# Performance work log

Hardware: AMD Instinct MI355X
Metric: run time of the kernel (lower is better)

The kernel has to match this reference:

```python
import jax, jax.numpy as jnp
import numpy as np


def _kernelize(data, projection_matrix):
    # FAVOR+ positive softmax features: ratio * h(x) * f(x @ P^T)
    # h(x) = exp(-||x||^2 / 2), f(u) = exp(u)
    d = data.shape[-1]
    r = projection_matrix.shape[0]
    data_norm = (d ** -0.25) * data                       # [n, d]
    ratio = r ** -0.5
    data_dash = jnp.einsum('id,rd->ir', data_norm, projection_matrix)  # [n, r]
    h = jnp.exp(-0.5 * jnp.sum(data_norm * data_norm, axis=-1, keepdims=True))  # [n, 1]
    return ratio * h * jnp.exp(data_dash)                 # [n, r]


def setup_inputs() -> dict:
    key = jax.random.key(0)
    k1, k2, k3, k4 = jax.random.split(key, 4)
    n, d, dv, r = 65536, 64, 64, 256
    q = jax.random.normal(k1, (n, d), dtype=jnp.float32)
    k = jax.random.normal(k2, (n, d), dtype=jnp.float32)
    v = jax.random.normal(k3, (n, dv), dtype=jnp.float32)
    projection_matrix = jax.random.normal(k4, (r, d), dtype=jnp.float32)
    return {"q": q, "k": k, "v": v, "projection_matrix": projection_matrix}


def reference(q, k, v, projection_matrix):
    q_hat = _kernelize(q, projection_matrix)              # [n, r]
    k_hat = _kernelize(k, projection_matrix)              # [n, r]
    z = k_hat.T @ v                                       # [r, dv]  (FAVOR associativity)
    w = q_hat @ z                                         # [n, dv]
    d_inv = 1.0 / jnp.sum(q_hat * jnp.sum(k_hat, axis=0), axis=1, keepdims=True)  # [n, 1]
    return d_inv * w
```

## Files before the change

### kernel.cpp

```cpp
#include <hip/hip_runtime.h>
#include <math.h>

typedef __attribute__((ext_vector_type(8))) short bf16x8;
typedef __attribute__((ext_vector_type(4))) short bf16x4;
typedef __attribute__((ext_vector_type(4))) float f32x4;

#define NROWS 65536
#define RFEAT 256
#define PARTN 20480
#define NGROUP 16

#define OFF_PB 0
#define OFF_ZB 32768
#define OFF_P2 73728
#define OFF_VB 1384448
#define OFF_PARTIALS 9773056

#define SC 0.35355339059327373f
#define LNRATIO -2.772588722239781f

__device__ __forceinline__ unsigned short f2bf(float f) {
    union { float f; unsigned int u; } v; v.f = f;
    unsigned int r = v.u + 0x7FFFu + ((v.u >> 16) & 1u);
    return (unsigned short)(r >> 16);
}

__global__ __launch_bounds__(256)
void prep_kernel(const float* __restrict__ V, const float* __restrict__ P,
                 unsigned short* __restrict__ Vb, unsigned short* __restrict__ Pb)
{
    const int t = threadIdx.x;
    if (blockIdx.x == 1024) {
        const int l = t & 63, g = t >> 6;
        for (int f = g * 8; f < g * 8 + 8; f++) {
            const int kstep = f >> 4, nt = f & 15;
            const float* src = P + (nt * 16 + (l & 15)) * 64 + kstep * 32 + (l >> 4) * 8;
            bf16x8 frag;
            #pragma unroll
            for (int j = 0; j < 8; j++) frag[j] = (short)f2bf(SC * src[j]);
            *(bf16x8*)(Pb + f * 512 + l * 8) = frag;
        }
        return;
    }
    __shared__ unsigned short vl[64 * 68];
    const int row = t >> 2, c0 = (t & 3) * 16;
    const float4* src = (const float4*)(V + ((size_t)blockIdx.x * 64 + row) * 64 + c0);
    unsigned short* dst = vl + row * 68 + c0;
    #pragma unroll
    for (int jj = 0; jj < 4; jj++) {
        float4 a = src[jj];
        dst[4*jj+0] = f2bf(a.x); dst[4*jj+1] = f2bf(a.y);
        dst[4*jj+2] = f2bf(a.z); dst[4*jj+3] = f2bf(a.w);
    }
    __syncthreads();
    const int l = t & 63;
    #pragma unroll
    for (int h = 0; h < 2; h++) {
        const int f = (t >> 6) * 2 + h;
        const int ks = f >> 2, nt = f & 3;
        const int kb = ks * 32 + (l >> 4) * 8, n = nt * 16 + (l & 15);
        bf16x8 fr;
        #pragma unroll
        for (int j = 0; j < 8; j++) fr[j] = vl[(kb + j) * 68 + n];
        *(bf16x8*)(Vb + (((size_t)blockIdx.x * 2 + ks) * 4 + nt) * 512 + l * 8) = fr;
    }
}

template<int LDP, bool TRANS>
__device__ __forceinline__ void phi_chunk(const float* __restrict__ X, int chunkBase,
                                          const unsigned short* __restrict__ Pb,
                                          unsigned short* phi_lds, float* rc)
{
    const int t = threadIdx.x, l = t & 63, w = t >> 6;
    const float* ar = X + (size_t)(chunkBase + 16 * w + (l & 15)) * 64 + (l >> 4) * 8;
    bf16x8 a0, a1;
    float ss = 0.f;
    #pragma unroll
    for (int j = 0; j < 8; j++) { float x = ar[j];      ss += x * x; a0[j] = (short)f2bf(x); }
    #pragma unroll
    for (int j = 0; j < 8; j++) { float x = ar[32 + j]; ss += x * x; a1[j] = (short)f2bf(x); }
    ss += __shfl_xor(ss, 16);
    ss += __shfl_xor(ss, 32);
    if (l < 16) rc[16 * w + l] = -0.5f * (SC * SC) * ss + LNRATIO;
    __syncthreads();
    #pragma unroll
    for (int nt = 0; nt < 16; nt++) {
        bf16x8 b0 = *(const bf16x8*)(Pb + nt * 512 + l * 8);
        bf16x8 b1 = *(const bf16x8*)(Pb + (16 + nt) * 512 + l * 8);
        f32x4 acc = (f32x4){0.f, 0.f, 0.f, 0.f};
        acc = __builtin_amdgcn_mfma_f32_16x16x32_bf16(a0, b0, acc, 0, 0, 0);
        acc = __builtin_amdgcn_mfma_f32_16x16x32_bf16(a1, b1, acc, 0, 0, 0);
        const int col = nt * 16 + (l & 15);
        const int r0 = 16 * w + (l >> 4) * 4;
        if (TRANS) {
            bf16x4 pk;
            #pragma unroll
            for (int reg = 0; reg < 4; reg++)
                pk[reg] = (short)f2bf(__expf(acc[reg] + rc[r0 + reg]));
            *(bf16x4*)(phi_lds + col * LDP + r0) = pk;
        } else {
            #pragma unroll
            for (int reg = 0; reg < 4; reg++)
                phi_lds[(r0 + reg) * LDP + col] = f2bf(__expf(acc[reg] + rc[r0 + reg]));
        }
    }
    __syncthreads();
}

__global__ __launch_bounds__(256, 2)
void kv_fused_kernel(const float* __restrict__ Kp, const unsigned short* __restrict__ Vb,
                     const unsigned short* __restrict__ Pb,
                     float* __restrict__ partials, int chunksPerBlock)
{
    __shared__ unsigned short phi_lds[RFEAT * 72];
    __shared__ float rc[64];
    const int t = threadIdx.x, l = t & 63, w = t >> 6;

    f32x4 acc[4][5];
    #pragma unroll
    for (int mt = 0; mt < 4; mt++)
        #pragma unroll
        for (int nt = 0; nt < 5; nt++) acc[mt][nt] = (f32x4){0.f, 0.f, 0.f, 0.f};

    bf16x8 ones;
    #pragma unroll
    for (int j = 0; j < 8; j++) ones[j] = (short)(((l & 15) == 0) ? 0x3F80 : 0);

    const int base = blockIdx.x * chunksPerBlock * 64;
    for (int c = 0; c < chunksPerBlock; c++) {
        const int cb = base + c * 64;
        bf16x8 vf[2][4];
        const size_t k32 = (size_t)(cb >> 5);
        #pragma unroll
        for (int ks = 0; ks < 2; ks++)
            #pragma unroll
            for (int nt = 0; nt < 4; nt++)
                vf[ks][nt] = *(const bf16x8*)(Vb + ((k32 + ks) * 4 + nt) * 512 + l * 8);

        phi_chunk<72, true>(Kp, cb, Pb, phi_lds, rc);

        #pragma unroll
        for (int ks = 0; ks < 2; ks++) {
            bf16x8 af[4];
            #pragma unroll
            for (int mt = 0; mt < 4; mt++)
                af[mt] = *(const bf16x8*)(phi_lds + (64 * w + mt * 16 + (l & 15)) * 72
                                          + ks * 32 + (l >> 4) * 8);
            #pragma unroll
            for (int mt = 0; mt < 4; mt++) {
                #pragma unroll
                for (int nt = 0; nt < 4; nt++)
                    acc[mt][nt] = __builtin_amdgcn_mfma_f32_16x16x32_bf16(af[mt], vf[ks][nt], acc[mt][nt], 0, 0, 0);
                acc[mt][4] = __builtin_amdgcn_mfma_f32_16x16x32_bf16(af[mt], ones, acc[mt][4], 0, 0, 0);
            }
        }
    }
    float* slot = partials + (size_t)blockIdx.x * PARTN;
    #pragma unroll
    for (int mt = 0; mt < 4; mt++)
        #pragma unroll
        for (int nt = 0; nt < 5; nt++)
            *(f32x4*)(slot + (((w * 4 + mt) * 5 + nt) << 8) + l * 4) = acc[mt][nt];
}

__global__ __launch_bounds__(256)
void reduce1_kernel(const float* __restrict__ partials, float* __restrict__ p2,
                    int slotsPerGroup)
{
    const int idx = blockIdx.x * 256 + threadIdx.x;
    const int g = blockIdx.y;
    const float* base = partials + (size_t)g * slotsPerGroup * PARTN + idx;
    float s0 = 0.f, s1 = 0.f, s2 = 0.f, s3 = 0.f;
    int b = 0;
    for (; b + 4 <= slotsPerGroup; b += 4) {
        s0 += base[(size_t)(b + 0) * PARTN];
        s1 += base[(size_t)(b + 1) * PARTN];
        s2 += base[(size_t)(b + 2) * PARTN];
        s3 += base[(size_t)(b + 3) * PARTN];
    }
    for (; b < slotsPerGroup; b++) s0 += base[(size_t)b * PARTN];
    p2[(size_t)g * PARTN + idx] = (s0 + s1) + (s2 + s3);
}

__global__ __launch_bounds__(256)
void reduce2_kernel(const float* __restrict__ p2, unsigned short* __restrict__ Zb, int ngroups)
{
    const int idx = blockIdx.x * 256 + threadIdx.x;
    float s = 0.f;
    for (int g = 0; g < ngroups; g++) s += p2[(size_t)g * PARTN + idx];
    const int tile = idx >> 8, rem = idx & 255;
    const int l = rem >> 2, reg = rem & 3;
    const int nt = tile % 5, wmt = tile / 5;
    const int w = wmt >> 2, mt = wmt & 3;
    const int m = 64 * w + 16 * mt + 4 * (l >> 4) + reg;
    const int n = 16 * nt + (l & 15);
    Zb[((m >> 3) * 80 + n) * 8 + (m & 7)] = f2bf(s);
}

__global__ __launch_bounds__(256, 4)
void q_out_kernel(const float* __restrict__ Q, const unsigned short* __restrict__ Pb,
                  const unsigned short* __restrict__ Zb, float* __restrict__ out)
{
    __shared__ unsigned short phi_lds[64 * 280];
    __shared__ float rc[64];
    const int t = threadIdx.x, l = t & 63, w = t >> 6;
    const int base = blockIdx.x * 64;

    phi_chunk<280, false>(Q, base, Pb, phi_lds, rc);

    f32x4 acc[5];
    #pragma unroll
    for (int nt = 0; nt < 5; nt++) acc[nt] = (f32x4){0.f, 0.f, 0.f, 0.f};

    #pragma unroll
    for (int ks = 0; ks < 8; ks++) {
        bf16x8 a = *(const bf16x8*)(phi_lds + (16 * w + (l & 15)) * 280 + ks * 32 + (l >> 4) * 8);
        #pragma unroll
        for (int nt = 0; nt < 5; nt++) {
            bf16x8 b = *(const bf16x8*)(Zb + ((ks * 4 + (l >> 4)) * 80 + nt * 16 + (l & 15)) * 8);
            acc[nt] = __builtin_amdgcn_mfma_f32_16x16x32_bf16(a, b, acc[nt], 0, 0, 0);
        }
    }
    float inv[4];
    #pragma unroll
    for (int reg = 0; reg < 4; reg++) {
        float den = __shfl(acc[4][reg], (l & 48));
        inv[reg] = 1.0f / den;
    }
    const int row = base + 16 * w + (l >> 4) * 4;
    #pragma unroll
    for (int nt = 0; nt < 4; nt++)
        #pragma unroll
        for (int reg = 0; reg < 4; reg++)
            out[(size_t)(row + reg) * 64 + nt * 16 + (l & 15)] = acc[nt][reg] * inv[reg];
}

extern "C" void kernel_launch(void* const* d_in, const int* in_sizes, int n_in,
                              void* d_out, int out_size, void* d_ws, size_t ws_size,
                              hipStream_t stream) {
    const float* q = (const float*)d_in[0];
    const float* k = (const float*)d_in[1];
    const float* v = (const float*)d_in[2];
    const float* P = (const float*)d_in[3];
    float* out = (float*)d_out;

    unsigned short* Pb = (unsigned short*)((char*)d_ws + OFF_PB);
    unsigned short* Zb = (unsigned short*)((char*)d_ws + OFF_ZB);
    float* p2          = (float*)((char*)d_ws + OFF_P2);
    unsigned short* Vb = (unsigned short*)((char*)d_ws + OFF_VB);
    float* partials    = (float*)((char*)d_ws + OFF_PARTIALS);

    long avail = ((long)ws_size - OFF_PARTIALS) / (long)(PARTN * 4);
    int NB = 256;
    while (NB > NGROUP && (long)NB > avail) NB >>= 1;
    int chunks = 1024 / NB;
    int ngroups = (NB >= NGROUP) ? NGROUP : NB;
    int spg = NB / ngroups;

    prep_kernel<<<1025, 256, 0, stream>>>(v, P, Vb, Pb);
    kv_fused_kernel<<<NB, 256, 0, stream>>>(k, Vb, Pb, partials, chunks);
    reduce1_kernel<<<dim3(80, ngroups), 256, 0, stream>>>(partials, p2, spg);
    reduce2_kernel<<<80, 256, 0, stream>>>(p2, Zb, ngroups);
    q_out_kernel<<<1024, 256, 0, stream>>>(q, Pb, Zb, out);
}
```

Before: 144.3 us.

## Prefetch two row chunks upfront and fix KV grid at 512 blocks

The K·V kernel now runs a fixed 512 blocks that each handle two 64-row chunks. Both chunks' raw K rows and V fragments are loaded into registers before any compute, so the global-load latency overlaps. The Q output kernel likewise processes two chunks per block, loading both chunks' Q rows upfront to hide load latency behind the first chunk's compute. This doubles the partials buffer and drops the workspace-size fallback, which risks overflowing a small workspace and adds register pressure.

```diff
diff --git a/kernel.cpp b/kernel.cpp
--- a/kernel.cpp
+++ b/kernel.cpp
@@ -5,10 +5,10 @@
 typedef __attribute__((ext_vector_type(4))) short bf16x4;
 typedef __attribute__((ext_vector_type(4))) float f32x4;
 
-#define NROWS 65536
 #define RFEAT 256
 #define PARTN 20480
 #define NGROUP 16
+#define NB_KV 512
 
 #define OFF_PB 0
 #define OFF_ZB 32768
@@ -18,6 +18,8 @@
 
 #define SC 0.35355339059327373f
 #define LNRATIO -2.772588722239781f
+
+struct Raw { float x[16]; };
 
 __device__ __forceinline__ unsigned short f2bf(float f) {
     union { float f; unsigned int u; } v; v.f = f;
@@ -66,19 +68,30 @@
     }
 }
 
+__device__ __forceinline__ Raw load_chunk(const float* __restrict__ X, int chunkBase,
+                                          int l, int w)
+{
+    const float* ar = X + (size_t)(chunkBase + 16 * w + (l & 15)) * 64 + (l >> 4) * 8;
+    Raw r;
+    #pragma unroll
+    for (int j = 0; j < 8; j++) r.x[j] = ar[j];
+    #pragma unroll
+    for (int j = 0; j < 8; j++) r.x[8 + j] = ar[32 + j];
+    return r;
+}
+
 template<int LDP, bool TRANS>
-__device__ __forceinline__ void phi_chunk(const float* __restrict__ X, int chunkBase,
-                                          const unsigned short* __restrict__ Pb,
-                                          unsigned short* phi_lds, float* rc)
-{
-    const int t = threadIdx.x, l = t & 63, w = t >> 6;
-    const float* ar = X + (size_t)(chunkBase + 16 * w + (l & 15)) * 64 + (l >> 4) * 8;
+__device__ __forceinline__ void phi_process(const Raw& r,
+                                            const unsigned short* __restrict__ Pb,
+                                            unsigned short* phi_lds, float* rc,
+                                            int l, int w)
+{
     bf16x8 a0, a1;
     float ss = 0.f;
     #pragma unroll
-    for (int j = 0; j < 8; j++) { float x = ar[j];      ss += x * x; a0[j] = (short)f2bf(x); }
-    #pragma unroll
-    for (int j = 0; j < 8; j++) { float x = ar[32 + j]; ss += x * x; a1[j] = (short)f2bf(x); }
+    for (int j = 0; j < 8; j++) { float x = r.x[j];     ss += x * x; a0[j] = (short)f2bf(x); }
+    #pragma unroll
+    for (int j = 0; j < 8; j++) { float x = r.x[8 + j]; ss += x * x; a1[j] = (short)f2bf(x); }
     ss += __shfl_xor(ss, 16);
     ss += __shfl_xor(ss, 32);
     if (l < 16) rc[16 * w + l] = -0.5f * (SC * SC) * ss + LNRATIO;
@@ -110,7 +123,7 @@
 __global__ __launch_bounds__(256, 2)
 void kv_fused_kernel(const float* __restrict__ Kp, const unsigned short* __restrict__ Vb,
                      const unsigned short* __restrict__ Pb,
-                     float* __restrict__ partials, int chunksPerBlock)
+                     float* __restrict__ partials)
 {
     __shared__ unsigned short phi_lds[RFEAT * 72];
     __shared__ float rc[64];
@@ -126,19 +139,25 @@
     #pragma unroll
     for (int j = 0; j < 8; j++) ones[j] = (short)(((l & 15) == 0) ? 0x3F80 : 0);
 
-    const int base = blockIdx.x * chunksPerBlock * 64;
-    for (int c = 0; c < chunksPerBlock; c++) {
-        const int cb = base + c * 64;
-        bf16x8 vf[2][4];
-        const size_t k32 = (size_t)(cb >> 5);
+    const int base = blockIdx.x * 128;
+
+    Raw raw0 = load_chunk(Kp, base, l, w);
+    Raw raw1 = load_chunk(Kp, base + 64, l, w);
+    bf16x8 vf0[2][4], vf1[2][4];
+    {
+        const size_t k32a = (size_t)(base >> 5), k32b = k32a + 2;
         #pragma unroll
         for (int ks = 0; ks < 2; ks++)
             #pragma unroll
-            for (int nt = 0; nt < 4; nt++)
-                vf[ks][nt] = *(const bf16x8*)(Vb + ((k32 + ks) * 4 + nt) * 512 + l * 8);
-
-        phi_chunk<72, true>(Kp, cb, Pb, phi_lds, rc);
-
+            for (int nt = 0; nt < 4; nt++) {
+                vf0[ks][nt] = *(const bf16x8*)(Vb + ((k32a + ks) * 4 + nt) * 512 + l * 8);
+                vf1[ks][nt] = *(const bf16x8*)(Vb + ((k32b + ks) * 4 + nt) * 512 + l * 8);
+            }
+    }
+
+    #pragma unroll
+    for (int c = 0; c < 2; c++) {
+        phi_process<72, true>(c ? raw1 : raw0, Pb, phi_lds, rc, l, w);
         #pragma unroll
         for (int ks = 0; ks < 2; ks++) {
             bf16x8 af[4];
@@ -150,11 +169,13 @@
             for (int mt = 0; mt < 4; mt++) {
                 #pragma unroll
                 for (int nt = 0; nt < 4; nt++)
-                    acc[mt][nt] = __builtin_amdgcn_mfma_f32_16x16x32_bf16(af[mt], vf[ks][nt], acc[mt][nt], 0, 0, 0);
+                    acc[mt][nt] = __builtin_amdgcn_mfma_f32_16x16x32_bf16(
+                        af[mt], c ? vf1[ks][nt] : vf0[ks][nt], acc[mt][nt], 0, 0, 0);
                 acc[mt][4] = __builtin_amdgcn_mfma_f32_16x16x32_bf16(af[mt], ones, acc[mt][4], 0, 0, 0);
             }
         }
     }
+
     float* slot = partials + (size_t)blockIdx.x * PARTN;
     #pragma unroll
     for (int mt = 0; mt < 4; mt++)
@@ -197,6 +218,37 @@
     Zb[((m >> 3) * 80 + n) * 8 + (m & 7)] = f2bf(s);
 }
 
+__device__ __forceinline__ void q_gemm_store(const unsigned short* phi_lds,
+                                             const unsigned short* __restrict__ Zb,
+                                             float* __restrict__ out, int base,
+                                             int l, int w)
+{
+    f32x4 acc[5];
+    #pragma unroll
+    for (int nt = 0; nt < 5; nt++) acc[nt] = (f32x4){0.f, 0.f, 0.f, 0.f};
+    #pragma unroll
+    for (int ks = 0; ks < 8; ks++) {
+        bf16x8 a = *(const bf16x8*)(phi_lds + (16 * w + (l & 15)) * 280 + ks * 32 + (l >> 4) * 8);
+        #pragma unroll
+        for (int nt = 0; nt < 5; nt++) {
+            bf16x8 b = *(const bf16x8*)(Zb + ((ks * 4 + (l >> 4)) * 80 + nt * 16 + (l & 15)) * 8);
+            acc[nt] = __builtin_amdgcn_mfma_f32_16x16x32_bf16(a, b, acc[nt], 0, 0, 0);
+        }
+    }
+    float inv[4];
+    #pragma unroll
+    for (int reg = 0; reg < 4; reg++) {
+        float den = __shfl(acc[4][reg], (l & 48));
+        inv[reg] = 1.0f / den;
+    }
+    const int row = base + 16 * w + (l >> 4) * 4;
+    #pragma unroll
+    for (int nt = 0; nt < 4; nt++)
+        #pragma unroll
+        for (int reg = 0; reg < 4; reg++)
+            out[(size_t)(row + reg) * 64 + nt * 16 + (l & 15)] = acc[nt][reg] * inv[reg];
+}
+
 __global__ __launch_bounds__(256, 4)
 void q_out_kernel(const float* __restrict__ Q, const unsigned short* __restrict__ Pb,
                   const unsigned short* __restrict__ Zb, float* __restrict__ out)
@@ -204,35 +256,16 @@
     __shared__ unsigned short phi_lds[64 * 280];
     __shared__ float rc[64];
     const int t = threadIdx.x, l = t & 63, w = t >> 6;
-    const int base = blockIdx.x * 64;
-
-    phi_chunk<280, false>(Q, base, Pb, phi_lds, rc);
-
-    f32x4 acc[5];
-    #pragma unroll
-    for (int nt = 0; nt < 5; nt++) acc[nt] = (f32x4){0.f, 0.f, 0.f, 0.f};
-
-    #pragma unroll
-    for (int ks = 0; ks < 8; ks++) {
-        bf16x8 a = *(const bf16x8*)(phi_lds + (16 * w + (l & 15)) * 280 + ks * 32 + (l >> 4) * 8);
-        #pragma unroll
-        for (int nt = 0; nt < 5; nt++) {
-            bf16x8 b = *(const bf16x8*)(Zb + ((ks * 4 + (l >> 4)) * 80 + nt * 16 + (l & 15)) * 8);
-            acc[nt] = __builtin_amdgcn_mfma_f32_16x16x32_bf16(a, b, acc[nt], 0, 0, 0);
-        }
-    }
-    float inv[4];
-    #pragma unroll
-    for (int reg = 0; reg < 4; reg++) {
-        float den = __shfl(acc[4][reg], (l & 48));
-        inv[reg] = 1.0f / den;
-    }
-    const int row = base + 16 * w + (l >> 4) * 4;
-    #pragma unroll
-    for (int nt = 0; nt < 4; nt++)
-        #pragma unroll
-        for (int reg = 0; reg < 4; reg++)
-            out[(size_t)(row + reg) * 64 + nt * 16 + (l & 15)] = acc[nt][reg] * inv[reg];
+    const int base = blockIdx.x * 128;
+
+    Raw raw0 = load_chunk(Q, base, l, w);
+    Raw raw1 = load_chunk(Q, base + 64, l, w);
+
+    phi_process<280, false>(raw0, Pb, phi_lds, rc, l, w);
+    q_gemm_store(phi_lds, Zb, out, base, l, w);
+    __syncthreads();
+    phi_process<280, false>(raw1, Pb, phi_lds, rc, l, w);
+    q_gemm_store(phi_lds, Zb, out, base + 64, l, w);
 }
 
 extern "C" void kernel_launch(void* const* d_in, const int* in_sizes, int n_in,
@@ -250,16 +283,9 @@
     unsigned short* Vb = (unsigned short*)((char*)d_ws + OFF_VB);
     float* partials    = (float*)((char*)d_ws + OFF_PARTIALS);
 
-    long avail = ((long)ws_size - OFF_PARTIALS) / (long)(PARTN * 4);
-    int NB = 256;
-    while (NB > NGROUP && (long)NB > avail) NB >>= 1;
-    int chunks = 1024 / NB;
-    int ngroups = (NB >= NGROUP) ? NGROUP : NB;
-    int spg = NB / ngroups;
-
     prep_kernel<<<1025, 256, 0, stream>>>(v, P, Vb, Pb);
-    kv_fused_kernel<<<NB, 256, 0, stream>>>(k, Vb, Pb, partials, chunks);
-    reduce1_kernel<<<dim3(80, ngroups), 256, 0, stream>>>(partials, p2, spg);
-    reduce2_kernel<<<80, 256, 0, stream>>>(p2, Zb, ngroups);
-    q_out_kernel<<<1024, 256, 0, stream>>>(q, Pb, Zb, out);
-}
+    kv_fused_kernel<<<NB_KV, 256, 0, stream>>>(k, Vb, Pb, partials);
+    reduce1_kernel<<<dim3(80, NGROUP), 256, 0, stream>>>(partials, p2, NB_KV / NGROUP);
+    reduce2_kernel<<<80, 256, 0, stream>>>(p2, Zb, NGROUP);
+    q_out_kernel<<<512, 256, 0, stream>>>(q, Pb, Zb, out);
+}
```

Result: no change. 142.0 us (-1.6%).
